# Kernel tuning notes

Measured on AMD Instinct MI355X. Metric: run time of the kernel, lower is better.

The kernel has to match this reference:

```python
import jax, jax.numpy as jnp
import numpy as np

ASPECT_RATIOS = jnp.array([0.5, 1.0, 2.0], dtype=jnp.float32)
SCALES = jnp.array([1.0, 2.0, 4.0, 8.0, 16.0], dtype=jnp.float32)
BASE_SIZE = 16
STRIDE = 16
NEG_OVERLAP = 0.3
POS_OVERLAP = 0.7
PADDING = 0.0
RPN_BATCH = 256
RPN_FG_FRACTION = 0.5


def _mkanchors(ws, hs, x_ctr, y_ctr):
    return jnp.stack([x_ctr - 0.5 * (ws - 1), y_ctr - 0.5 * (hs - 1),
                      x_ctr + 0.5 * (ws - 1), y_ctr + 0.5 * (hs - 1)], axis=-1)


def _base_anchors():
    w = h = float(BASE_SIZE)
    x_ctr = y_ctr = 0.5 * (BASE_SIZE - 1)
    size = w * h
    size_ratios = size / ASPECT_RATIOS
    ws = jnp.round(jnp.sqrt(size_ratios))
    hs = jnp.round(ws * ASPECT_RATIOS)
    ratio_anchors = _mkanchors(ws, hs, x_ctr, y_ctr)          # (R,4)
    rw = ratio_anchors[:, 2] - ratio_anchors[:, 0] + 1
    rh = ratio_anchors[:, 3] - ratio_anchors[:, 1] + 1
    rx = ratio_anchors[:, 0] + 0.5 * (rw - 1)
    ry = ratio_anchors[:, 1] + 0.5 * (rh - 1)
    ws2 = rw[:, None] * SCALES[None, :]                        # (R,S)
    hs2 = rh[:, None] * SCALES[None, :]
    anchors = _mkanchors(ws2, hs2, rx[:, None], ry[:, None])   # (R,S,4)
    return anchors.reshape(-1, 4)                              # (A=R*S,4)


def _shifted_anchors(r, c):
    base = _base_anchors()                                     # (A,4)
    sx = jnp.arange(c, dtype=jnp.float32) * STRIDE
    sy = jnp.arange(r, dtype=jnp.float32) * STRIDE
    SX, SY = jnp.meshgrid(sx, sy)                              # (r,c)
    shifts = jnp.stack([SX.ravel(), SY.ravel(), SX.ravel(), SY.ravel()], axis=1)
    return (shifts[:, None, :] + base[None, :, :]).reshape(-1, 4)  # (K=r*c*A,4)


def _iou(a, b):
    area_a = (a[:, 2] - a[:, 0] + 1) * (a[:, 3] - a[:, 1] + 1)
    area_b = (b[:, 2] - b[:, 0] + 1) * (b[:, 3] - b[:, 1] + 1)
    iw = jnp.minimum(a[:, None, 2], b[None, :, 2]) - jnp.maximum(a[:, None, 0], b[None, :, 0]) + 1
    ih = jnp.minimum(a[:, None, 3], b[None, :, 3]) - jnp.maximum(a[:, None, 1], b[None, :, 1]) + 1
    inter = jnp.maximum(iw, 0) * jnp.maximum(ih, 0)
    return inter / (area_a[:, None] + area_b[None, :] - inter)


def _bbox_transform(ex, gt):
    ew = ex[:, 2] - ex[:, 0] + 1.0
    eh = ex[:, 3] - ex[:, 1] + 1.0
    ecx = ex[:, 0] + 0.5 * ew
    ecy = ex[:, 1] + 0.5 * eh
    gw = gt[:, 2] - gt[:, 0] + 1.0
    gh = gt[:, 3] - gt[:, 1] + 1.0
    gcx = gt[:, 0] + 0.5 * gw
    gcy = gt[:, 1] + 0.5 * gh
    return jnp.stack([(gcx - ecx) / ew, (gcy - ecy) / eh,
                      jnp.log(gw / ew), jnp.log(gh / eh)], axis=1)


def reference(target_bounding_boxes, metadata, scores):
    meta = metadata[0]
    gt = target_bounding_boxes[0]                               # (G,4)
    r, c = scores.shape[1], scores.shape[2]
    anchors = _shifted_anchors(r, c)                            # (K,4)
    K = anchors.shape[0]
    h, w = meta[0], meta[1]

    # anchors fully inside the image (padding=0); outside anchors masked
    inside = ((anchors[:, 0] >= -PADDING) & (anchors[:, 1] >= -PADDING) &
              (anchors[:, 2] < w + PADDING) & (anchors[:, 3] < h + PADDING))

    clipped = jnp.stack([jnp.clip(anchors[:, 0], 0.0, w - 1),
                         jnp.clip(anchors[:, 1], 0.0, h - 1),
                         jnp.clip(anchors[:, 2], 0.0, w - 1),
                         jnp.clip(anchors[:, 3], 0.0, h - 1)], axis=1)

    overlaps = _iou(clipped, gt)                                # (K,G)
    overlaps = jnp.where(inside[:, None], overlaps, -1.0)       # ignore outside anchors
    argmax_overlaps = jnp.argmax(overlaps, axis=1)              # best gt per anchor
    max_overlaps = jnp.max(overlaps, axis=1)
    gt_argmax = jnp.argmax(overlaps, axis=0)                    # best anchor per gt

    labels = jnp.full((K,), -1.0, dtype=jnp.float32)
    labels = jnp.where(inside & (max_overlaps < NEG_OVERLAP), 0.0, labels)
    labels = labels.at[gt_argmax].set(1.0)                      # dedup handled by .set
    labels = jnp.where(inside & (max_overlaps >= POS_OVERLAP), 1.0, labels)
    labels = jnp.where(inside, labels, -1.0)                    # unmap fill=-1

    # deterministic subsampling (original shuffles randomly): keep first-by-index
    num_fg = int(RPN_FG_FRACTION * RPN_BATCH)
    pos = labels == 1.0
    pos_rank = jnp.cumsum(pos.astype(jnp.int32))
    labels = jnp.where(pos & (pos_rank > num_fg), -1.0, labels)
    num_pos = jnp.minimum(pos.sum(), num_fg)
    num_bg = RPN_BATCH - num_pos
    neg = labels == 0.0
    neg_rank = jnp.cumsum(neg.astype(jnp.int32))
    labels = jnp.where(neg & (neg_rank > num_bg), -1.0, labels)

    matched_gt = gt[argmax_overlaps]                            # (K,4) gather
    bbox_targets = _bbox_transform(clipped, matched_gt)
    bbox_targets = jnp.where(inside[:, None], bbox_targets, 0.0)  # unmap fill=0

    return anchors[None], bbox_targets[None], labels[None]


def setup_inputs() -> dict:
    key = jax.random.key(0)
    k1, k2 = jax.random.split(key)
    H = W = 1600
    G = 100
    r = c = H // STRIDE                                          # 100
    A = 15                                                       # 3 ratios * 5 scales
    xy = jax.random.uniform(k1, (G, 2), minval=0.0, maxval=1400.0)
    wh = jax.random.uniform(k2, (G, 2), minval=16.0, maxval=200.0)
    gt = jnp.concatenate([xy, xy + wh], axis=1)[None]            # (1,G,4)
    metadata = jnp.array([[float(H), float(W), 1.0]], dtype=jnp.float32)
    scores = jnp.zeros((1, r, c, A), dtype=jnp.float32)          # only shape is used
    return {"target_bounding_boxes": gt, "metadata": metadata, "scores": scores}
```

## Files before the change

### kernel.cpp

```cpp
#include <hip/hip_runtime.h>
#include <math.h>


#define NUM_A 15
#define NUM_FG 128
#define RPN_BATCH 256
#define BLOCK 256
#define MAXG 256
#define MAXNB 1024

__device__ __forceinline__ void base_anchor(int a, float& bx1, float& by1,
                                            float& bx2, float& by2) {
    const float RW[3] = {23.f, 16.f, 11.f};
    const float RH[3] = {12.f, 16.f, 22.f};
    int i = a / 5;
    int j = a - i * 5;
    float sc = (float)(1 << j);
    float w = RW[i] * sc;
    float h = RH[i] * sc;
    bx1 = 7.5f - 0.5f * (w - 1.f);
    by1 = 7.5f - 0.5f * (h - 1.f);
    bx2 = 7.5f + 0.5f * (w - 1.f);
    by2 = 7.5f + 0.5f * (h - 1.f);
}

__device__ __forceinline__ void anchor_coords(int k, int c, float& x1, float& y1,
                                              float& x2, float& y2) {
    int a = k % NUM_A;
    int p = k / NUM_A;
    int xi = p % c;
    int yi = p / c;
    float bx1, by1, bx2, by2;
    base_anchor(a, bx1, by1, bx2, by2);
    float sx = (float)xi * 16.f;
    float sy = (float)yi * 16.f;
    x1 = sx + bx1;  y1 = sy + by1;
    x2 = sx + bx2;  y2 = sy + by2;
}

__device__ __forceinline__ unsigned long long packvk(float v, int k) {
    unsigned u = __float_as_uint(v);
    u = (u & 0x80000000u) ? ~u : (u | 0x80000000u);
    return ((unsigned long long)u << 32) | (unsigned)(~k);
}

__global__ void __launch_bounds__(BLOCK) k_main(
        const float* __restrict__ gt, const float* __restrict__ meta,
        float* __restrict__ out_anch, float* __restrict__ out_bb,
        float* __restrict__ lab0, int* __restrict__ posc, int* __restrict__ negc,
        unsigned long long* __restrict__ bestg, int K, int c, int G) {
    __shared__ float4 s_gt[MAXG];
    __shared__ unsigned long long s_best[MAXG];
    __shared__ int swp[4], swn[4];
    int tid = threadIdx.x;
    int lane = tid & 63, wid = tid >> 6;
    const float4* gtv = (const float4*)gt;
    for (int g = tid; g < G; g += BLOCK) {
        s_gt[g] = gtv[g];
        s_best[g] = 0ULL;
    }
    __syncthreads();

    int k = blockIdx.x * BLOCK + tid;
    bool valid = (k < K);
    float h = meta[0], w = meta[1];
    float wm1 = __fsub_rn(w, 1.f), hm1 = __fsub_rn(h, 1.f);

    float x1, y1, x2, y2;
    anchor_coords(k, c, x1, y1, x2, y2);
    if (valid) ((float4*)out_anch)[k] = make_float4(x1, y1, x2, y2);
    bool inside = (x1 >= 0.f) && (y1 >= 0.f) && (x2 < w) && (y2 < h);
    bool act_anchor = valid && inside;

    float cx1 = fminf(fmaxf(x1, 0.f), wm1);
    float cy1 = fminf(fmaxf(y1, 0.f), hm1);
    float cx2 = fminf(fmaxf(x2, 0.f), wm1);
    float cy2 = fminf(fmaxf(y2, 0.f), hm1);
    float area_a = __fmul_rn(__fadd_rn(__fsub_rn(cx2, cx1), 1.f),
                             __fadd_rn(__fsub_rn(cy2, cy1), 1.f));

    float wx1 = cx1, wy1 = cy1, wx2 = cx2, wy2 = cy2;
    #pragma unroll
    for (int off = 1; off < 64; off <<= 1) {
        wx1 = fminf(wx1, __shfl_xor(wx1, off, 64));
        wy1 = fminf(wy1, __shfl_xor(wy1, off, 64));
        wx2 = fmaxf(wx2, __shfl_xor(wx2, off, 64));
        wy2 = fmaxf(wy2, __shfl_xor(wy2, off, 64));
    }

    float maxv = 0.f;
    int arg = 0;
    if (__any(act_anchor ? 1 : 0)) {
        for (int g = 0; g < G; ++g) {
            float4 gb = gtv[g];
            float ox = __fadd_rn(__fsub_rn(fminf(wx2, gb.z), fmaxf(wx1, gb.x)), 1.f);
            float oy = __fadd_rn(__fsub_rn(fminf(wy2, gb.w), fmaxf(wy1, gb.y)), 1.f);
            if (!__any((ox > 0.f && oy > 0.f) ? 1 : 0)) continue;

            float gw = __fadd_rn(__fsub_rn(gb.z, gb.x), 1.f);
            float gh = __fadd_rn(__fsub_rn(gb.w, gb.y), 1.f);
            float areab = __fmul_rn(gw, gh);
            float iw = __fadd_rn(__fsub_rn(fminf(cx2, gb.z), fmaxf(cx1, gb.x)), 1.f);
            float ih = __fadd_rn(__fsub_rn(fminf(cy2, gb.w), fmaxf(cy1, gb.y)), 1.f);
            float inter = __fmul_rn(fmaxf(iw, 0.f), fmaxf(ih, 0.f));
            float v = 0.f;
            if (act_anchor && inter > 0.f) {
                float denom = __fsub_rn(__fadd_rn(area_a, areab), inter);
                v = __fdiv_rn(inter, denom);
                atomicMax(&s_best[g], packvk(v, k));
            }
            if (v > maxv) { maxv = v; arg = g; }
        }
    }
    __syncthreads();
    for (int g = tid; g < G; g += BLOCK)
        if (s_best[g] != 0ULL) atomicMax(&bestg[g], s_best[g]);

    float labf = -1.f;
    if (valid) {
        float t0 = 0.f, t1 = 0.f, t2 = 0.f, t3 = 0.f;
        if (inside) {
            labf = (maxv >= 0.7f) ? 1.f : (maxv < 0.3f ? 0.f : -1.f);
            float4 gb = s_gt[arg];
            float ew  = __fadd_rn(__fsub_rn(cx2, cx1), 1.f);
            float eh  = __fadd_rn(__fsub_rn(cy2, cy1), 1.f);
            float ecx = __fadd_rn(cx1, __fmul_rn(0.5f, ew));
            float ecy = __fadd_rn(cy1, __fmul_rn(0.5f, eh));
            float gw  = __fadd_rn(__fsub_rn(gb.z, gb.x), 1.f);
            float gh  = __fadd_rn(__fsub_rn(gb.w, gb.y), 1.f);
            float gcx = __fadd_rn(gb.x, __fmul_rn(0.5f, gw));
            float gcy = __fadd_rn(gb.y, __fmul_rn(0.5f, gh));
            t0 = __fdiv_rn(__fsub_rn(gcx, ecx), ew);
            t1 = __fdiv_rn(__fsub_rn(gcy, ecy), eh);
            t2 = logf(__fdiv_rn(gw, ew));
            t3 = logf(__fdiv_rn(gh, eh));
        }
        ((float4*)out_bb)[k] = make_float4(t0, t1, t2, t3);
        lab0[k] = labf;
    }

    bool pos = valid && (labf == 1.f);
    bool neg = valid && (labf == 0.f);
    unsigned long long bp = __ballot(pos ? 1 : 0);
    unsigned long long bn = __ballot(neg ? 1 : 0);
    if (lane == 0) { swp[wid] = __popcll(bp); swn[wid] = __popcll(bn); }
    __syncthreads();
    if (tid == 0) {
        posc[blockIdx.x] = swp[0] + swp[1] + swp[2] + swp[3];
        negc[blockIdx.x] = swn[0] + swn[1] + swn[2] + swn[3];
    }
}

__global__ void __launch_bounds__(BLOCK) k_finish(
        const float* __restrict__ lab0, float* __restrict__ out_lab,
        const int* __restrict__ posc, const int* __restrict__ negc,
        const unsigned long long* __restrict__ bestg, int K, int NB, int G) {
    __shared__ int s_p[MAXNB], s_n[MAXNB];
    __shared__ int s_cp[BLOCK], s_cn[BLOCK];
    __shared__ int s_k[MAXG];
    __shared__ unsigned char s_over[BLOCK];
    __shared__ int swp[4], swn[4];
    int tid = threadIdx.x;
    int lane = tid & 63, wid = tid >> 6;

    for (int i = tid; i < MAXNB; i += BLOCK) {
        s_p[i] = (i < NB) ? posc[i] : 0;
        s_n[i] = (i < NB) ? negc[i] : 0;
    }
    s_over[tid] = 0;
    int kstar = -1;
    if (tid < G) {
        unsigned long long u = bestg[tid];
        if (u != 0ULL)
            kstar = (int)(~(unsigned)(u & 0xffffffffu));
    }
    if (tid < MAXG) s_k[tid] = kstar;
    __syncthreads();
    bool mine = (kstar >= 0);
    if (mine) {
        for (int j = 0; j < tid; ++j)
            if (s_k[j] == kstar) { mine = false; break; }
    }
    if (mine) {
        int b = kstar / BLOCK;
        float oldl = lab0[kstar];
        if (oldl != 1.f) {
            atomicAdd(&s_p[b], 1);
            if (oldl == 0.f) atomicAdd(&s_n[b], -1);
        }
        if (b == (int)blockIdx.x) s_over[kstar - b * BLOCK] = 1;
    }
    __syncthreads();

    int base = tid * 4;
    int p0 = s_p[base], p1 = s_p[base + 1], p2 = s_p[base + 2], p3 = s_p[base + 3];
    int n0 = s_n[base], n1 = s_n[base + 1], n2 = s_n[base + 2], n3 = s_n[base + 3];
    int sump = p0 + p1 + p2 + p3, sumn = n0 + n1 + n2 + n3;
    s_cp[tid] = sump; s_cn[tid] = sumn;
    __syncthreads();
    int vp = sump, vn = sumn;
    for (int off = 1; off < BLOCK; off <<= 1) {
        int ap = 0, an = 0;
        if (tid >= off) { ap = s_cp[tid - off]; an = s_cn[tid - off]; }
        __syncthreads();
        vp += ap; vn += an;
        s_cp[tid] = vp; s_cn[tid] = vn;
        __syncthreads();
    }
    int ep = vp - sump, en = vn - sumn;
    s_p[base] = ep; ep += p0; s_p[base + 1] = ep; ep += p1;
    s_p[base + 2] = ep; ep += p2; s_p[base + 3] = ep;
    s_n[base] = en; en += n0; s_n[base + 1] = en; en += n1;
    s_n[base + 2] = en; en += n2; s_n[base + 3] = en;
    __syncthreads();
    int total_pos = s_cp[BLOCK - 1];
    int np = total_pos < NUM_FG ? total_pos : NUM_FG;
    int nbg = RPN_BATCH - np;

    int k = blockIdx.x * BLOCK + tid;
    bool valid = (k < K);
    float lv = -1.f;
    if (valid) lv = s_over[tid] ? 1.f : lab0[k];
    bool posf = valid && (lv == 1.f);
    bool negf = valid && (lv == 0.f);
    unsigned long long lm = (1ULL << lane) - 1ULL;
    unsigned long long bp2 = __ballot(posf ? 1 : 0);
    unsigned long long bn2 = __ballot(negf ? 1 : 0);
    if (lane == 0) { swp[wid] = __popcll(bp2); swn[wid] = __popcll(bn2); }
    __syncthreads();
    int poff = 0, noff = 0;
    for (int wv = 0; wv < wid; ++wv) { poff += swp[wv]; noff += swn[wv]; }
    int prank = s_p[blockIdx.x] + poff + __popcll(bp2 & lm) + 1;
    int nrank = s_n[blockIdx.x] + noff + __popcll(bn2 & lm) + 1;
    if (valid) {
        float outv = lv;
        if (posf && prank > NUM_FG) outv = -1.f;
        if (negf && nrank > nbg)    outv = -1.f;
        out_lab[k] = outv;
    }
}

extern "C" void kernel_launch(void* const* d_in, const int* in_sizes, int n_in,
                              void* d_out, int out_size, void* d_ws, size_t ws_size,
                              hipStream_t stream) {
    const float* gt   = (const float*)d_in[0];
    const float* meta = (const float*)d_in[1];
    int G  = in_sizes[0] / 4;
    int rc = in_sizes[2] / NUM_A;
    int c = 1;
    while ((long long)(c + 1) * (c + 1) <= (long long)rc) ++c;
    int K  = rc * NUM_A;
    int NB = (K + BLOCK - 1) / BLOCK;

    float* out      = (float*)d_out;
    float* out_anch = out;
    float* out_bb   = out + (size_t)4 * K;
    float* out_lab  = out + (size_t)8 * K;

    unsigned long long* bestg = (unsigned long long*)d_ws;
    int* posc  = (int*)(bestg + MAXG);
    int* negc  = posc + MAXNB;
    float* lab0 = (float*)(negc + MAXNB);

    hipMemsetAsync(bestg, 0, MAXG * sizeof(unsigned long long), stream);
    hipLaunchKernelGGL(k_main, dim3(NB), dim3(BLOCK), 0, stream,
                       gt, meta, out_anch, out_bb, lab0, posc, negc, bestg, K, c, G);
    hipLaunchKernelGGL(k_finish, dim3(NB), dim3(BLOCK), 0, stream,
                       lab0, out_lab, posc, negc, bestg, K, NB, G);
}
```

Baseline: 109.2 us.

## Cull GT boxes per block into shared list before IoU loop

Each block now computes a conservative bounding box of all its anchors from hardcoded anchor extents and compacts the GT boxes that overlap it into a shared-memory list. The per-anchor IoU loop then walks only that list, with no per-iteration wave vote and no global GT reads, and inactive anchors skip the loop entirely. The finish kernel loads the per-block counts with int4 vector loads. This adds a shared atomic compaction step, and because the list order is nondeterministic, ties are broken explicitly on the lower GT index. The vector loads assume the count buffers are padded to a multiple of 1024 entries.

```diff
diff --git a/kernel.cpp b/kernel.cpp
--- a/kernel.cpp
+++ b/kernel.cpp
@@ -8,6 +8,11 @@
 #define BLOCK 256
 #define MAXG 256
 #define MAXNB 1024
+
+#define EXT_X1 (-176.f)
+#define EXT_X2 (191.f)
+#define EXT_Y1 (-168.f)
+#define EXT_Y2 (183.f)
 
 __device__ __forceinline__ void base_anchor(int a, float& bx1, float& by1,
                                             float& bx2, float& by2) {
@@ -50,66 +55,81 @@
         float* __restrict__ lab0, int* __restrict__ posc, int* __restrict__ negc,
         unsigned long long* __restrict__ bestg, int K, int c, int G) {
     __shared__ float4 s_gt[MAXG];
+    __shared__ float4 s_gtc[MAXG];
+    __shared__ int s_gidx[MAXG];
     __shared__ unsigned long long s_best[MAXG];
+    __shared__ int s_nl;
     __shared__ int swp[4], swn[4];
     int tid = threadIdx.x;
     int lane = tid & 63, wid = tid >> 6;
     const float4* gtv = (const float4*)gt;
+
+    float h = meta[0], w = meta[1];
+    float wm1 = __fsub_rn(w, 1.f), hm1 = __fsub_rn(h, 1.f);
+
+    int k0 = blockIdx.x * BLOCK;
+    int k1 = min(k0 + BLOCK - 1, K - 1);
+    int p0 = k0 / NUM_A, p1 = k1 / NUM_A;
+    int y0 = p0 / c, y1 = p1 / c;
+    int xm0, xm1;
+    if (y0 == y1) { xm0 = p0 - y0 * c; xm1 = p1 - y1 * c; }
+    else          { xm0 = 0;           xm1 = c - 1; }
+    float bbx1 = fminf(fmaxf((float)(xm0 * 16) + EXT_X1, 0.f), wm1);
+    float bbx2 = fminf(fmaxf((float)(xm1 * 16) + EXT_X2, 0.f), wm1);
+    float bby1 = fminf(fmaxf((float)(y0 * 16) + EXT_Y1, 0.f), hm1);
+    float bby2 = fminf(fmaxf((float)(y1 * 16) + EXT_Y2, 0.f), hm1);
+
+    if (tid == 0) s_nl = 0;
+    for (int g = tid; g < G; g += BLOCK) s_best[g] = 0ULL;
+    __syncthreads();
     for (int g = tid; g < G; g += BLOCK) {
-        s_gt[g] = gtv[g];
-        s_best[g] = 0ULL;
-    }
-    __syncthreads();
+        float4 gb = gtv[g];
+        s_gt[g] = gb;
+        float ox = __fadd_rn(__fsub_rn(fminf(bbx2, gb.z), fmaxf(bbx1, gb.x)), 1.f);
+        float oy = __fadd_rn(__fsub_rn(fminf(bby2, gb.w), fmaxf(bby1, gb.y)), 1.f);
+        if (ox > 0.f && oy > 0.f) {
+            int slot = atomicAdd(&s_nl, 1);
+            s_gtc[slot] = gb;
+            s_gidx[slot] = g;
+        }
+    }
+    __syncthreads();
+    int NL = s_nl;
 
     int k = blockIdx.x * BLOCK + tid;
     bool valid = (k < K);
-    float h = meta[0], w = meta[1];
-    float wm1 = __fsub_rn(w, 1.f), hm1 = __fsub_rn(h, 1.f);
-
-    float x1, y1, x2, y2;
-    anchor_coords(k, c, x1, y1, x2, y2);
-    if (valid) ((float4*)out_anch)[k] = make_float4(x1, y1, x2, y2);
-    bool inside = (x1 >= 0.f) && (y1 >= 0.f) && (x2 < w) && (y2 < h);
+
+    float x1, y1f, x2, y2f;
+    anchor_coords(k, c, x1, y1f, x2, y2f);
+    if (valid) ((float4*)out_anch)[k] = make_float4(x1, y1f, x2, y2f);
+    bool inside = (x1 >= 0.f) && (y1f >= 0.f) && (x2 < w) && (y2f < h);
     bool act_anchor = valid && inside;
 
     float cx1 = fminf(fmaxf(x1, 0.f), wm1);
-    float cy1 = fminf(fmaxf(y1, 0.f), hm1);
+    float cy1 = fminf(fmaxf(y1f, 0.f), hm1);
     float cx2 = fminf(fmaxf(x2, 0.f), wm1);
-    float cy2 = fminf(fmaxf(y2, 0.f), hm1);
+    float cy2 = fminf(fmaxf(y2f, 0.f), hm1);
     float area_a = __fmul_rn(__fadd_rn(__fsub_rn(cx2, cx1), 1.f),
                              __fadd_rn(__fsub_rn(cy2, cy1), 1.f));
 
-    float wx1 = cx1, wy1 = cy1, wx2 = cx2, wy2 = cy2;
-    #pragma unroll
-    for (int off = 1; off < 64; off <<= 1) {
-        wx1 = fminf(wx1, __shfl_xor(wx1, off, 64));
-        wy1 = fminf(wy1, __shfl_xor(wy1, off, 64));
-        wx2 = fmaxf(wx2, __shfl_xor(wx2, off, 64));
-        wy2 = fmaxf(wy2, __shfl_xor(wy2, off, 64));
-    }
-
     float maxv = 0.f;
     int arg = 0;
-    if (__any(act_anchor ? 1 : 0)) {
-        for (int g = 0; g < G; ++g) {
-            float4 gb = gtv[g];
-            float ox = __fadd_rn(__fsub_rn(fminf(wx2, gb.z), fmaxf(wx1, gb.x)), 1.f);
-            float oy = __fadd_rn(__fsub_rn(fminf(wy2, gb.w), fmaxf(wy1, gb.y)), 1.f);
-            if (!__any((ox > 0.f && oy > 0.f) ? 1 : 0)) continue;
-
+    if (act_anchor) {
+        for (int i = 0; i < NL; ++i) {
+            float4 gb = s_gtc[i];
+            int g = s_gidx[i];
             float gw = __fadd_rn(__fsub_rn(gb.z, gb.x), 1.f);
             float gh = __fadd_rn(__fsub_rn(gb.w, gb.y), 1.f);
             float areab = __fmul_rn(gw, gh);
             float iw = __fadd_rn(__fsub_rn(fminf(cx2, gb.z), fmaxf(cx1, gb.x)), 1.f);
             float ih = __fadd_rn(__fsub_rn(fminf(cy2, gb.w), fmaxf(cy1, gb.y)), 1.f);
             float inter = __fmul_rn(fmaxf(iw, 0.f), fmaxf(ih, 0.f));
-            float v = 0.f;
-            if (act_anchor && inter > 0.f) {
+            if (inter > 0.f) {
                 float denom = __fsub_rn(__fadd_rn(area_a, areab), inter);
-                v = __fdiv_rn(inter, denom);
+                float v = __fdiv_rn(inter, denom);
                 atomicMax(&s_best[g], packvk(v, k));
+                if (v > maxv || (v == maxv && g < arg)) { maxv = v; arg = g; }
             }
-            if (v > maxv) { maxv = v; arg = g; }
         }
     }
     __syncthreads();
@@ -162,11 +182,17 @@
     __shared__ int swp[4], swn[4];
     int tid = threadIdx.x;
     int lane = tid & 63, wid = tid >> 6;
-
-    for (int i = tid; i < MAXNB; i += BLOCK) {
-        s_p[i] = (i < NB) ? posc[i] : 0;
-        s_n[i] = (i < NB) ? negc[i] : 0;
-    }
+    int base = tid * 4;
+
+    int4 pv = ((const int4*)posc)[tid];
+    int4 nv = ((const int4*)negc)[tid];
+    if (base + 0 >= NB) pv.x = 0;  if (base + 1 >= NB) pv.y = 0;
+    if (base + 2 >= NB) pv.z = 0;  if (base + 3 >= NB) pv.w = 0;
+    if (base + 0 >= NB) nv.x = 0;  if (base + 1 >= NB) nv.y = 0;
+    if (base + 2 >= NB) nv.z = 0;  if (base + 3 >= NB) nv.w = 0;
+    ((int4*)s_p)[tid] = pv;
+    ((int4*)s_n)[tid] = nv;
+
     s_over[tid] = 0;
     int kstar = -1;
     if (tid < G) {
@@ -192,7 +218,6 @@
     }
     __syncthreads();
 
-    int base = tid * 4;
     int p0 = s_p[base], p1 = s_p[base + 1], p2 = s_p[base + 2], p3 = s_p[base + 3];
     int n0 = s_n[base], n1 = s_n[base + 1], n2 = s_n[base + 2], n3 = s_n[base + 3];
     int sump = p0 + p1 + p2 + p3, sumn = n0 + n1 + n2 + n3;
```

Measured after the change: 101.8 us (median of 2 runs). 6.8% less time.
